# Optimization experiments

Measured on AMD Instinct MI355X. Metric: run time of the kernel, lower is better.

The kernel has to match this reference:

```python
import jax, jax.numpy as jnp
import numpy as np

N_NODES = 50000
N_EDGES = 800000
IN_DIM = 1024
HID = 512          # hidden_channels * heads, heads=1
N_CLASSES = 6
N_GRAPHS = 8
NEG_SLOPE = 0.2    # PyG GATConv default LeakyReLU slope
EPS = 1e-16


def gat_conv(x, W, att_src, att_dst, bias, src, dst):
    """PyG GATConv with heads=1, concat=True.
    x: [N, Fin], W: [Fin, C], att_src/att_dst: [C], bias: [C],
    src/dst: [E] (edge_index[0], edge_index[1]); messages flow src -> dst.
    """
    h = x @ W                                   # [N, C]
    a_s = h @ att_src                           # [N]
    a_d = h @ att_dst                           # [N]
    e = jax.nn.leaky_relu(a_s[src] + a_d[dst], NEG_SLOPE)   # [E]
    # segment softmax over destination node
    m = jax.ops.segment_max(e, dst, num_segments=N_NODES)   # [N]
    ex = jnp.exp(e - m[dst])                                 # [E]
    denom = jax.ops.segment_sum(ex, dst, num_segments=N_NODES)  # [N]
    alpha = ex / (denom[dst] + EPS)                           # [E]
    msg = alpha[:, None] * h[src]                             # [E, C]
    out = jax.ops.segment_sum(msg, dst, num_segments=N_NODES)  # [N, C]
    return out + bias


def setup_inputs() -> dict:
    key = jax.random.key(0)
    ks = jax.random.split(key, 20)
    x = jax.random.normal(ks[0], (N_NODES, IN_DIM), dtype=jnp.float32)
    edge_index = jax.random.randint(ks[1], (2, N_EDGES), 0, N_NODES, dtype=jnp.int32)
    batch = jnp.sort(jax.random.randint(ks[2], (N_NODES,), 0, N_GRAPHS, dtype=jnp.int32))

    def glorot(k, shape):
        fan = shape[0] + shape[-1]
        return jax.random.normal(k, shape, dtype=jnp.float32) * jnp.sqrt(2.0 / fan)

    inp = {"x": x, "edge_index": edge_index, "batch": batch}
    dims = [(IN_DIM, HID), (HID, HID), (HID, HID)]
    for i, (fi, fo) in enumerate(dims, start=1):
        inp[f"W{i}"] = glorot(ks[3 * i], (fi, fo))
        inp[f"as{i}"] = glorot(ks[3 * i + 1], (fo,))
        inp[f"ad{i}"] = glorot(ks[3 * i + 2], (fo,))
        inp[f"b{i}"] = jnp.zeros((fo,), dtype=jnp.float32)
    inp["Wlin"] = glorot(ks[13], (HID, N_CLASSES))
    inp["blin"] = jnp.zeros((N_CLASSES,), dtype=jnp.float32)
    return inp


def reference(x, W1, as1, ad1, b1, W2, as2, ad2, b2, W3, as3, ad3, b3,
              Wlin, blin, edge_index, batch):
    src, dst = edge_index[0], edge_index[1]
    h = gat_conv(x, W1, as1, ad1, b1, src, dst)
    h = jax.nn.relu(h)
    h = gat_conv(h, W2, as2, ad2, b2, src, dst)
    h = jax.nn.relu(h)
    h = gat_conv(h, W3, as3, ad3, b3, src, dst)
    # global_max_pool over graphs; dropout is identity in eval mode
    pooled = jax.ops.segment_max(h, batch, num_segments=N_GRAPHS)  # [G, HID]
    return pooled @ Wlin + blin                                     # [G, num_classes]
```

## Files before the change

### kernel.cpp

```cpp
#include <hip/hip_runtime.h>
#include <cmath>

#define N_NODES 50000
#define N_EDGES 800000
#define IN_DIM 1024
#define HID 512
#define N_CLASSES 6
#define N_GRAPHS 8
#define NEG_SLOPE 0.2f
#define SCAN_BLK 256
#define N_SCAN_BLOCKS ((N_NODES + SCAN_BLK - 1) / SCAN_BLK)
#define POOL_STRIP 256
#define POOL_NBLOCKS ((N_NODES + POOL_STRIP - 1) / POOL_STRIP)

typedef _Float16 half8 __attribute__((ext_vector_type(8)));
typedef _Float16 half4 __attribute__((ext_vector_type(4)));
typedef float floatx4 __attribute__((ext_vector_type(4)));

typedef const __attribute__((address_space(1))) void* gas_ptr;
typedef __attribute__((address_space(3))) void* las_ptr;
#define GLOAD16(gp, lp) \
    __builtin_amdgcn_global_load_lds((gas_ptr)(gp), (las_ptr)(lp), 16, 0, 0)

__global__ __launch_bounds__(256) void cast_x_f16(const float* __restrict__ x,
                                                  _Float16* __restrict__ x16) {
    const size_t TOT = (size_t)N_NODES * IN_DIM;
    size_t i = ((size_t)blockIdx.x * blockDim.x + threadIdx.x) * 8;
    const size_t step = (size_t)gridDim.x * blockDim.x * 8;
    for (; i < TOT; i += step) {
        float4 f0 = *(const float4*)(x + i);
        float4 f1 = *(const float4*)(x + i + 4);
        half8 o;
        o[0] = (_Float16)f0.x; o[1] = (_Float16)f0.y;
        o[2] = (_Float16)f0.z; o[3] = (_Float16)f0.w;
        o[4] = (_Float16)f1.x; o[5] = (_Float16)f1.y;
        o[6] = (_Float16)f1.z; o[7] = (_Float16)f1.w;
        *(half8*)(x16 + i) = o;
    }
}

__global__ __launch_bounds__(256) void transpose_cast_W(const float* __restrict__ W,
                                                        _Float16* __restrict__ Wt,
                                                        int K) {
    __shared__ float sh[32][33];
    const int kb = blockIdx.x * 32, nb = blockIdx.y * 32;
    const int tx = threadIdx.x & 31, ty = threadIdx.x >> 5;
#pragma unroll
    for (int i = 0; i < 32; i += 8)
        sh[ty + i][tx] = W[(size_t)(kb + ty + i) * HID + nb + tx];
    __syncthreads();
#pragma unroll
    for (int i = 0; i < 32; i += 8)
        Wt[(size_t)(nb + ty + i) * K + kb + tx] = (_Float16)sh[tx][ty + i];
}

__global__ __launch_bounds__(256) void gemm_mfma_f16(const _Float16* __restrict__ A,
                                                     const _Float16* __restrict__ Bt,
                                                     _Float16* __restrict__ C,
                                                     int M, int K) {
    const int nwg = gridDim.x;
    const int bid = blockIdx.x;
    const int q = nwg >> 3, r = nwg & 7;
    const int xcd = bid & 7, local = bid >> 3;
    const int wgid = (xcd < r) ? xcd * (q + 1) + local
                               : r * (q + 1) + (xcd - r) * q + local;
    const int rowBase = (wgid >> 2) * 128;
    const int colBase = (wgid & 3) * 128;

    const int tid  = threadIdx.x;
    const int lane = tid & 63;
    const int wave = tid >> 6;
    const int wm = wave >> 1, wn = wave & 1;

    __shared__ __align__(16) _Float16 As[128 * 64];
    __shared__ __align__(16) _Float16 Bs[128 * 64];

    const int fr = lane & 15;
    const int kc = lane >> 4;

    floatx4 acc[4][4] = {};

    const int lrow   = lane >> 3;
    const int gchunk = ((lane & 7) ^ lrow) * 8;
    const _Float16* aS[4];
    const _Float16* bS[4];
    _Float16* aD[4];
    _Float16* bD[4];
#pragma unroll
    for (int i = 0; i < 4; ++i) {
        int rr = wave * 32 + i * 8;
        int ar = rowBase + rr + lrow; if (ar > M - 1) ar = M - 1;
        aS[i] = A  + (size_t)ar * K + gchunk;
        bS[i] = Bt + (size_t)(colBase + rr + lrow) * K + gchunk;
        aD[i] = As + rr * 64;
        bD[i] = Bs + rr * 64;
    }

    const int cp0 = ((kc)     ^ (fr & 7)) * 8;
    const int cp1 = ((4 + kc) ^ (fr & 7)) * 8;
    const int aro = (wm * 64 + fr) * 64;
    const int bro = (wn * 64 + fr) * 64;

    for (int kb = 0; kb < K; kb += 64) {
#pragma unroll
        for (int i = 0; i < 4; ++i) {
            GLOAD16(aS[i] + kb, aD[i]);
            GLOAD16(bS[i] + kb, bD[i]);
        }
        __syncthreads();

#pragma unroll
        for (int kks = 0; kks < 2; ++kks) {
            const int cp = kks ? cp1 : cp0;
            half8 afr[4], bfr[4];
#pragma unroll
            for (int mi = 0; mi < 4; ++mi)
                afr[mi] = *(const half8*)&As[aro + mi * 1024 + cp];
#pragma unroll
            for (int ni = 0; ni < 4; ++ni)
                bfr[ni] = *(const half8*)&Bs[bro + ni * 1024 + cp];
#pragma unroll
            for (int mi = 0; mi < 4; ++mi)
#pragma unroll
                for (int ni = 0; ni < 4; ++ni)
                    acc[mi][ni] = __builtin_amdgcn_mfma_f32_16x16x32_f16(
                        afr[mi], bfr[ni], acc[mi][ni], 0, 0, 0);
        }
        __syncthreads();
    }

#pragma unroll
    for (int mi = 0; mi < 4; ++mi) {
#pragma unroll
        for (int ni = 0; ni < 4; ++ni) {
            int col = colBase + wn * 64 + ni * 16 + fr;
#pragma unroll
            for (int j = 0; j < 4; ++j) {
                int row = rowBase + wm * 64 + mi * 16 + kc * 4 + j;
                if (row < M) C[(size_t)row * HID + col] = (_Float16)acc[mi][ni][j];
            }
        }
    }
}

__global__ __launch_bounds__(256) void adot_kernel(const _Float16* __restrict__ h,
                                                   const float* __restrict__ att_s,
                                                   const float* __restrict__ att_d,
                                                   float* __restrict__ a_s,
                                                   float* __restrict__ a_d) {
    int wave = threadIdx.x >> 6;
    int lane = threadIdx.x & 63;
    int n = blockIdx.x * 4 + wave;
    if (n >= N_NODES) return;
    half8 hv = *(const half8*)(h + (size_t)n * HID + lane * 8);
    float4 s0 = ((const float4*)att_s)[lane * 2];
    float4 s1 = ((const float4*)att_s)[lane * 2 + 1];
    float4 d0 = ((const float4*)att_d)[lane * 2];
    float4 d1 = ((const float4*)att_d)[lane * 2 + 1];
    float hf[8];
#pragma unroll
    for (int q = 0; q < 8; ++q) hf[q] = (float)hv[q];
    float ss = hf[0]*s0.x + hf[1]*s0.y + hf[2]*s0.z + hf[3]*s0.w
             + hf[4]*s1.x + hf[5]*s1.y + hf[6]*s1.z + hf[7]*s1.w;
    float sd = hf[0]*d0.x + hf[1]*d0.y + hf[2]*d0.z + hf[3]*d0.w
             + hf[4]*d1.x + hf[5]*d1.y + hf[6]*d1.z + hf[7]*d1.w;
#pragma unroll
    for (int off = 32; off; off >>= 1) {
        ss += __shfl_down(ss, off);
        sd += __shfl_down(sd, off);
    }
    if (lane == 0) { a_s[n] = ss; a_d[n] = sd; }
}

__global__ void count_kernel(const int* __restrict__ dst, int* __restrict__ cnt) {
    int i = blockIdx.x * blockDim.x + threadIdx.x;
    if (i < N_EDGES) atomicAdd(cnt + dst[i], 1);
}

__global__ __launch_bounds__(SCAN_BLK) void scan1_kernel(const int* __restrict__ cnt,
                                                         int* __restrict__ partial,
                                                         int* __restrict__ blocksum) {
    __shared__ int tmp[SCAN_BLK];
    int t = threadIdx.x;
    int i = blockIdx.x * SCAN_BLK + t;
    int v = (i < N_NODES) ? cnt[i] : 0;
    tmp[t] = v;
    __syncthreads();
    for (int off = 1; off < SCAN_BLK; off <<= 1) {
        int u = (t >= off) ? tmp[t - off] : 0;
        __syncthreads();
        tmp[t] += u;
        __syncthreads();
    }
    if (i < N_NODES) partial[i] = tmp[t] - v;
    if (t == SCAN_BLK - 1) blocksum[blockIdx.x] = tmp[t];
}

__global__ __launch_bounds__(SCAN_BLK) void scan2_kernel(int* __restrict__ blocksum) {
    __shared__ int tmp[SCAN_BLK];
    int t = threadIdx.x;
    int v = (t < N_SCAN_BLOCKS) ? blocksum[t] : 0;
    tmp[t] = v;
    __syncthreads();
    for (int off = 1; off < SCAN_BLK; off <<= 1) {
        int u = (t >= off) ? tmp[t - off] : 0;
        __syncthreads();
        tmp[t] += u;
        __syncthreads();
    }
    if (t < N_SCAN_BLOCKS) blocksum[t] = tmp[t] - v;
}

__global__ __launch_bounds__(SCAN_BLK) void scan3_kernel(const int* __restrict__ partial,
                                                         const int* __restrict__ blocksum,
                                                         int* __restrict__ rowptr,
                                                         int* __restrict__ cursor) {
    int i = blockIdx.x * SCAN_BLK + threadIdx.x;
    if (i < N_NODES) {
        int r = partial[i] + blocksum[blockIdx.x];
        rowptr[i] = r;
        cursor[i] = r;
    }
    if (i == 0) rowptr[N_NODES] = N_EDGES;
}

__global__ void scatter_kernel(const int* __restrict__ src, const int* __restrict__ dst,
                               int* __restrict__ cursor, int* __restrict__ src_s) {
    int i = blockIdx.x * blockDim.x + threadIdx.x;
    if (i >= N_EDGES) return;
    int p = atomicAdd(cursor + dst[i], 1);
    src_s[p] = src[i];
}

__global__ __launch_bounds__(256) void aggregate_fused(const int* __restrict__ rowptr,
                                                       const int* __restrict__ src_s,
                                                       const float* __restrict__ a_s,
                                                       const float* __restrict__ a_d,
                                                       const _Float16* __restrict__ h,
                                                       const float* __restrict__ bias,
                                                       int do_relu,
                                                       _Float16* __restrict__ outx) {
    int wave = threadIdx.x >> 6;
    int lane = threadIdx.x & 63;
    int n = blockIdx.x * 4 + wave;
    if (n >= N_NODES) return;
    int beg = rowptr[n], end = rowptr[n + 1];
    float a_dn = a_d[n];
    float m = -__builtin_inff();
    float ssum = 0.f;
    float acc[8] = {};
    for (int j = beg; j < end; ++j) {
        int s = src_s[j];
        float v = a_s[s] + a_dn;
        v = v > 0.f ? v : NEG_SLOPE * v;
        float mn = fmaxf(m, v);
        float scale = __expf(m - mn);
        float p = __expf(v - mn);
        ssum = ssum * scale + p;
        m = mn;
        half8 hv = *(const half8*)(h + (size_t)s * HID + lane * 8);
#pragma unroll
        for (int q = 0; q < 8; ++q)
            acc[q] = fmaf(p, (float)hv[q], acc[q] * scale);
    }
    float inv = 1.f / (ssum + 1e-16f);
    const float4 b0 = ((const float4*)(bias + lane * 8))[0];
    const float4 b1 = ((const float4*)(bias + lane * 8))[1];
    float o[8];
    o[0] = acc[0] * inv + b0.x; o[1] = acc[1] * inv + b0.y;
    o[2] = acc[2] * inv + b0.z; o[3] = acc[3] * inv + b0.w;
    o[4] = acc[4] * inv + b1.x; o[5] = acc[5] * inv + b1.y;
    o[6] = acc[6] * inv + b1.z; o[7] = acc[7] * inv + b1.w;
    half8 ov;
#pragma unroll
    for (int q = 0; q < 8; ++q) {
        float val = do_relu ? fmaxf(o[q], 0.f) : o[q];
        ov[q] = (_Float16)val;
    }
    *(half8*)(outx + (size_t)n * HID + lane * 8) = ov;
}

__global__ __launch_bounds__(128) void pool1_kernel(const _Float16* __restrict__ X,
                                                    const int* __restrict__ batch,
                                                    float* __restrict__ partial) {
    const int t = threadIdx.x;
    const int b = blockIdx.x;
    const int n0 = b * POOL_STRIP;
    const int n1 = min(n0 + POOL_STRIP, N_NODES);
    const float NEG = -__builtin_inff();
    const float4 neg4 = make_float4(NEG, NEG, NEG, NEG);
#pragma unroll
    for (int g = 0; g < N_GRAPHS; ++g)
        ((float4*)(partial + ((size_t)b * N_GRAPHS + g) * HID))[t] = neg4;
    int gcur = batch[n0];
    float4 m = neg4;
    for (int n = n0; n < n1; ++n) {
        int g = batch[n];
        if (g != gcur) {
            ((float4*)(partial + ((size_t)b * N_GRAPHS + gcur) * HID))[t] = m;
            m = neg4;
            gcur = g;
        }
        half4 hv = *(const half4*)(X + (size_t)n * HID + t * 4);
        m.x = fmaxf(m.x, (float)hv[0]); m.y = fmaxf(m.y, (float)hv[1]);
        m.z = fmaxf(m.z, (float)hv[2]); m.w = fmaxf(m.w, (float)hv[3]);
    }
    ((float4*)(partial + ((size_t)b * N_GRAPHS + gcur) * HID))[t] = m;
}

__global__ __launch_bounds__(128) void pool2_kernel(const float* __restrict__ partial,
                                                    float* __restrict__ pooled) {
    const int g = blockIdx.x;
    const int t = threadIdx.x;
    const float NEG = -__builtin_inff();
    float4 m = make_float4(NEG, NEG, NEG, NEG);
    for (int b = 0; b < POOL_NBLOCKS; ++b) {
        float4 v = ((const float4*)(partial + ((size_t)b * N_GRAPHS + g) * HID))[t];
        m.x = fmaxf(m.x, v.x); m.y = fmaxf(m.y, v.y);
        m.z = fmaxf(m.z, v.z); m.w = fmaxf(m.w, v.w);
    }
    ((float4*)(pooled + (size_t)g * HID))[t] = m;
}

__global__ __launch_bounds__(64) void final_linear_kernel(const float* __restrict__ pooled,
                                                          const float* __restrict__ Wlin,
                                                          const float* __restrict__ blin,
                                                          float* __restrict__ out) {
    int t = threadIdx.x;
    if (t >= N_GRAPHS * N_CLASSES) return;
    int g = t / N_CLASSES, c = t % N_CLASSES;
    float s = blin[c];
    for (int k = 0; k < HID; ++k)
        s = fmaf(pooled[(size_t)g * HID + k], Wlin[(size_t)k * N_CLASSES + c], s);
    out[t] = s;
}

extern "C" void kernel_launch(void* const* d_in, const int* in_sizes, int n_in,
                              void* d_out, int out_size, void* d_ws, size_t ws_size,
                              hipStream_t stream) {
    const float* x       = (const float*)d_in[0];
    const int*   eidx    = (const int*)d_in[1];
    const int*   batch   = (const int*)d_in[2];
    const float* W[3]    = {(const float*)d_in[3], (const float*)d_in[7], (const float*)d_in[11]};
    const float* Asrc[3] = {(const float*)d_in[4], (const float*)d_in[8], (const float*)d_in[12]};
    const float* Adst[3] = {(const float*)d_in[5], (const float*)d_in[9], (const float*)d_in[13]};
    const float* Bias[3] = {(const float*)d_in[6], (const float*)d_in[10], (const float*)d_in[14]};
    const float* Wlin    = (const float*)d_in[15];
    const float* blin    = (const float*)d_in[16];
    const int* src = eidx;
    const int* dst = eidx + N_EDGES;

    float* wsf    = (float*)d_ws;
    _Float16* x16 = (_Float16*)wsf;
    _Float16* hH  = (_Float16*)(wsf + 25600000);
    _Float16* xAct= (_Float16*)(wsf + 25600000 + 12800000);
    float* a_s    = wsf + 25600000 + 12800000 + 12800000;
    float* a_d    = a_s + N_NODES;
    float* pooled = a_d + N_NODES;
    int* cnt      = (int*)(pooled + N_GRAPHS * HID);
    int* rowptr   = cnt + N_NODES;
    int* cursor   = rowptr + N_NODES + 1;
    int* partial  = cursor + N_NODES;
    int* blocksum = partial + N_NODES;
    int* src_s    = blocksum + 256;
    _Float16* Wt  = (_Float16*)(src_s + N_EDGES);

    int edge_blocks = (N_EDGES + 255) / 256;

    hipMemsetAsync(cnt, 0, N_NODES * sizeof(int), stream);
    count_kernel<<<edge_blocks, 256, 0, stream>>>(dst, cnt);
    scan1_kernel<<<N_SCAN_BLOCKS, SCAN_BLK, 0, stream>>>(cnt, partial, blocksum);
    scan2_kernel<<<1, SCAN_BLK, 0, stream>>>(blocksum);
    scan3_kernel<<<N_SCAN_BLOCKS, SCAN_BLK, 0, stream>>>(partial, blocksum, rowptr, cursor);
    scatter_kernel<<<edge_blocks, 256, 0, stream>>>(src, dst, cursor, src_s);

    cast_x_f16<<<2048, 256, 0, stream>>>(x, x16);

    const int nrow_tiles = (N_NODES + 127) / 128;
    const int gemm_blocks = nrow_tiles * (HID / 128);
    for (int l = 0; l < 3; ++l) {
        int K = (l == 0) ? IN_DIM : HID;
        dim3 tgrid(K / 32, HID / 32);
        transpose_cast_W<<<tgrid, 256, 0, stream>>>(W[l], Wt, K);
        const _Float16* Ain = (l == 0) ? x16 : xAct;
        gemm_mfma_f16<<<gemm_blocks, 256, 0, stream>>>(Ain, Wt, hH, N_NODES, K);
        adot_kernel<<<(N_NODES + 3) / 4, 256, 0, stream>>>(hH, Asrc[l], Adst[l], a_s, a_d);
        aggregate_fused<<<(N_NODES + 3) / 4, 256, 0, stream>>>(
            rowptr, src_s, a_s, a_d, hH, Bias[l], (l < 2) ? 1 : 0, xAct);
    }

    float* pool_partial = (float*)x16;
    pool1_kernel<<<POOL_NBLOCKS, 128, 0, stream>>>(xAct, batch, pool_partial);
    pool2_kernel<<<N_GRAPHS, 128, 0, stream>>>(pool_partial, pooled);
    final_linear_kernel<<<1, 64, 0, stream>>>(pooled, Wlin, blin, (float*)d_out);
}
```

Measured before the change: 840.0 us.

## Split edge softmax into a separate alpha kernel and simplify the aggregation loop

The per-node online softmax is moved out of the feature-aggregation kernel into a new kernel. It computes normalized attention weights per edge, using 16 lanes per node with shuffle reductions. Aggregation then becomes a plain weighted gather-sum, unrolled by two, so more row loads are in flight and the per-edge exp calls and rescale chain disappear. The three weight transposes are also batched into one launch before the layer loop. The cost is an extra pass that writes and reads an edge-sized alpha buffer, which reuses the no-longer-needed part of the x16 workspace.

```diff
diff --git a/kernel.cpp b/kernel.cpp
--- a/kernel.cpp
+++ b/kernel.cpp
@@ -39,9 +39,17 @@
     }
 }
 
-__global__ __launch_bounds__(256) void transpose_cast_W(const float* __restrict__ W,
-                                                        _Float16* __restrict__ Wt,
-                                                        int K) {
+__global__ __launch_bounds__(256) void transpose_cast_W3(const float* __restrict__ W1,
+                                                         const float* __restrict__ W2,
+                                                         const float* __restrict__ W3,
+                                                         _Float16* __restrict__ Wt1,
+                                                         _Float16* __restrict__ Wt2,
+                                                         _Float16* __restrict__ Wt3) {
+    const int l = blockIdx.z;
+    const float* W = (l == 0) ? W1 : (l == 1) ? W2 : W3;
+    _Float16* Wt   = (l == 0) ? Wt1 : (l == 1) ? Wt2 : Wt3;
+    const int K    = (l == 0) ? IN_DIM : HID;
+    if (blockIdx.x * 32 >= K) return;
     __shared__ float sh[32][33];
     const int kb = blockIdx.x * 32, nb = blockIdx.y * 32;
     const int tx = threadIdx.x & 31, ty = threadIdx.x >> 5;
@@ -232,45 +240,79 @@
     src_s[p] = src[i];
 }
 
-__global__ __launch_bounds__(256) void aggregate_fused(const int* __restrict__ rowptr,
-                                                       const int* __restrict__ src_s,
-                                                       const float* __restrict__ a_s,
-                                                       const float* __restrict__ a_d,
-                                                       const _Float16* __restrict__ h,
-                                                       const float* __restrict__ bias,
-                                                       int do_relu,
-                                                       _Float16* __restrict__ outx) {
+__global__ __launch_bounds__(256) void alpha_kernel(const int* __restrict__ rowptr,
+                                                    const int* __restrict__ src_s,
+                                                    const float* __restrict__ a_s,
+                                                    const float* __restrict__ a_d,
+                                                    float* __restrict__ alpha) {
+    const int grp = threadIdx.x >> 4;
+    const int l16 = threadIdx.x & 15;
+    const int n = blockIdx.x * 16 + grp;
+    if (n >= N_NODES) return;
+    const int beg = rowptr[n], end = rowptr[n + 1];
+    const float a_dn = a_d[n];
+
+    float vmax = -__builtin_inff();
+    for (int j = beg + l16; j < end; j += 16) {
+        float v = a_s[src_s[j]] + a_dn;
+        v = v > 0.f ? v : NEG_SLOPE * v;
+        alpha[j] = v;
+        vmax = fmaxf(vmax, v);
+    }
+#pragma unroll
+    for (int m = 1; m < 16; m <<= 1) vmax = fmaxf(vmax, __shfl_xor(vmax, m));
+
+    float psum = 0.f;
+    for (int j = beg + l16; j < end; j += 16) {
+        float p = __expf(alpha[j] - vmax);
+        alpha[j] = p;
+        psum += p;
+    }
+#pragma unroll
+    for (int m = 1; m < 16; m <<= 1) psum += __shfl_xor(psum, m);
+
+    const float inv = 1.f / (psum + 1e-16f);
+    for (int j = beg + l16; j < end; j += 16) alpha[j] *= inv;
+}
+
+__global__ __launch_bounds__(256) void aggregate2(const int* __restrict__ rowptr,
+                                                  const int* __restrict__ src_s,
+                                                  const float* __restrict__ alpha,
+                                                  const _Float16* __restrict__ h,
+                                                  const float* __restrict__ bias,
+                                                  int do_relu,
+                                                  _Float16* __restrict__ outx) {
     int wave = threadIdx.x >> 6;
     int lane = threadIdx.x & 63;
     int n = blockIdx.x * 4 + wave;
     if (n >= N_NODES) return;
-    int beg = rowptr[n], end = rowptr[n + 1];
-    float a_dn = a_d[n];
-    float m = -__builtin_inff();
-    float ssum = 0.f;
+    const int beg = rowptr[n], end = rowptr[n + 1];
     float acc[8] = {};
-    for (int j = beg; j < end; ++j) {
-        int s = src_s[j];
-        float v = a_s[s] + a_dn;
-        v = v > 0.f ? v : NEG_SLOPE * v;
-        float mn = fmaxf(m, v);
-        float scale = __expf(m - mn);
-        float p = __expf(v - mn);
-        ssum = ssum * scale + p;
-        m = mn;
-        half8 hv = *(const half8*)(h + (size_t)s * HID + lane * 8);
-#pragma unroll
-        for (int q = 0; q < 8; ++q)
-            acc[q] = fmaf(p, (float)hv[q], acc[q] * scale);
-    }
-    float inv = 1.f / (ssum + 1e-16f);
+    int j = beg;
+    for (; j + 1 < end; j += 2) {
+        int s0 = src_s[j], s1 = src_s[j + 1];
+        float al0 = alpha[j], al1 = alpha[j + 1];
+        half8 hv0 = *(const half8*)(h + (size_t)s0 * HID + lane * 8);
+        half8 hv1 = *(const half8*)(h + (size_t)s1 * HID + lane * 8);
+#pragma unroll
+        for (int q = 0; q < 8; ++q) acc[q] = fmaf(al0, (float)hv0[q], acc[q]);
+#pragma unroll
+        for (int q = 0; q < 8; ++q) acc[q] = fmaf(al1, (float)hv1[q], acc[q]);
+    }
+    if (j < end) {
+        int s0 = src_s[j];
+        float al0 = alpha[j];
+        half8 hv0 = *(const half8*)(h + (size_t)s0 * HID + lane * 8);
+#pragma unroll
+        for (int q = 0; q < 8; ++q) acc[q] = fmaf(al0, (float)hv0[q], acc[q]);
+    }
     const float4 b0 = ((const float4*)(bias + lane * 8))[0];
     const float4 b1 = ((const float4*)(bias + lane * 8))[1];
     float o[8];
-    o[0] = acc[0] * inv + b0.x; o[1] = acc[1] * inv + b0.y;
-    o[2] = acc[2] * inv + b0.z; o[3] = acc[3] * inv + b0.w;
-    o[4] = acc[4] * inv + b1.x; o[5] = acc[5] * inv + b1.y;
-    o[6] = acc[6] * inv + b1.z; o[7] = acc[7] * inv + b1.w;
+    o[0] = acc[0] + b0.x; o[1] = acc[1] + b0.y;
+    o[2] = acc[2] + b0.z; o[3] = acc[3] + b0.w;
+    o[4] = acc[4] + b1.x; o[5] = acc[5] + b1.y;
+    o[6] = acc[6] + b1.z; o[7] = acc[7] + b1.w;
     half8 ov;
 #pragma unroll
     for (int q = 0; q < 8; ++q) {
@@ -352,6 +394,7 @@
 
     float* wsf    = (float*)d_ws;
     _Float16* x16 = (_Float16*)wsf;
+    float* ealpha = wsf + 24800000;
     _Float16* hH  = (_Float16*)(wsf + 25600000);
     _Float16* xAct= (_Float16*)(wsf + 25600000 + 12800000);
     float* a_s    = wsf + 25600000 + 12800000 + 12800000;
@@ -363,7 +406,10 @@
     int* partial  = cursor + N_NODES;
     int* blocksum = partial + N_NODES;
     int* src_s    = blocksum + 256;
-    _Float16* Wt  = (_Float16*)(src_s + N_EDGES);
+    _Float16* Wt1 = (_Float16*)(src_s + N_EDGES);
+    _Float16* Wt2 = Wt1 + (size_t)HID * IN_DIM;
+    _Float16* Wt3 = Wt2 + (size_t)HID * HID;
+    _Float16* WtL[3] = {Wt1, Wt2, Wt3};
 
     int edge_blocks = (N_EDGES + 255) / 256;
 
@@ -375,18 +421,19 @@
     scatter_kernel<<<edge_blocks, 256, 0, stream>>>(src, dst, cursor, src_s);
 
     cast_x_f16<<<2048, 256, 0, stream>>>(x, x16);
+    dim3 tgrid(IN_DIM / 32, HID / 32, 3);
+    transpose_cast_W3<<<tgrid, 256, 0, stream>>>(W[0], W[1], W[2], Wt1, Wt2, Wt3);
 
     const int nrow_tiles = (N_NODES + 127) / 128;
     const int gemm_blocks = nrow_tiles * (HID / 128);
     for (int l = 0; l < 3; ++l) {
         int K = (l == 0) ? IN_DIM : HID;
-        dim3 tgrid(K / 32, HID / 32);
-        transpose_cast_W<<<tgrid, 256, 0, stream>>>(W[l], Wt, K);
         const _Float16* Ain = (l == 0) ? x16 : xAct;
-        gemm_mfma_f16<<<gemm_blocks, 256, 0, stream>>>(Ain, Wt, hH, N_NODES, K);
+        gemm_mfma_f16<<<gemm_blocks, 256, 0, stream>>>(Ain, WtL[l], hH, N_NODES, K);
         adot_kernel<<<(N_NODES + 3) / 4, 256, 0, stream>>>(hH, Asrc[l], Adst[l], a_s, a_d);
-        aggregate_fused<<<(N_NODES + 3) / 4, 256, 0, stream>>>(
-            rowptr, src_s, a_s, a_d, hH, Bias[l], (l < 2) ? 1 : 0, xAct);
+        alpha_kernel<<<(N_NODES + 15) / 16, 256, 0, stream>>>(rowptr, src_s, a_s, a_d, ealpha);
+        aggregate2<<<(N_NODES + 3) / 4, 256, 0, stream>>>(
+            rowptr, src_s, ealpha, hH, Bias[l], (l < 2) ? 1 : 0, xAct);
     }
 
     float* pool_partial = (float*)x16;
```

After: 830.3 us. Within noise of the previous version (-1.2%).
